# Kernel tuning notes

Measured on AMD Instinct MI355X. Metric: run time of the kernel, lower is better.

The kernel has to match this reference:

```python
import jax, jax.numpy as jnp
import numpy as np

# Model dims (Llama-7B-like with GQA)
HID = 4096      # hidden_size
NH = 32         # query heads
NKV = 8         # kv heads
D = HID // NH   # head_dim = 128
S = 64          # num decode sequences (one token each)
NB = 4096       # num cache blocks
BS = 16         # block size
MC = 1024       # max context length
THETA = 10000.0 # rope base


def _rope(x, positions):
    # x: [S, h, D]; neox-style rotary over full head_dim
    half = D // 2
    inv_freq = 1.0 / (THETA ** (jnp.arange(half, dtype=jnp.float32) * 2.0 / D))
    ang = positions.astype(jnp.float32)[:, None] * inv_freq  # [S, half]
    cos = jnp.cos(ang)[:, None, :]
    sin = jnp.sin(ang)[:, None, :]
    x1, x2 = x[..., :half], x[..., half:]
    return jnp.concatenate([x1 * cos - x2 * sin, x2 * cos + x1 * sin], axis=-1)


def setup_inputs() -> dict:
    key = jax.random.key(0)
    ks = jax.random.split(key, 8)
    hidden_states = jax.random.normal(ks[0], (S, HID), dtype=jnp.float32)
    k_cache = jax.random.normal(ks[1], (NB, BS, NKV, D), dtype=jnp.float32)
    v_cache = jax.random.normal(ks[2], (NB, BS, NKV, D), dtype=jnp.float32)
    qkv_w = jax.random.normal(ks[3], ((NH + 2 * NKV) * D, HID), dtype=jnp.float32) * 0.02
    o_w = jax.random.normal(ks[4], (HID, NH * D), dtype=jnp.float32) * 0.02
    context_lens = jnp.clip(jax.random.randint(ks[5], (S,), 1, MC + 1), 1, MC).astype(jnp.int32)
    positions = (context_lens - 1).astype(jnp.int32)  # current token position
    block_tables = jax.random.randint(ks[6], (S, MC // BS), 0, NB).astype(jnp.int32)
    return {"hidden_states": hidden_states, "k_cache": k_cache, "v_cache": v_cache,
            "qkv_w": qkv_w, "o_w": o_w, "positions": positions,
            "context_lens": context_lens, "block_tables": block_tables}


def reference(hidden_states, k_cache, v_cache, qkv_w, o_w, positions, context_lens, block_tables):
    # QKV projection (no bias)
    qkv = hidden_states @ qkv_w.T  # [S, (NH+2*NKV)*D]
    q, k, v = jnp.split(qkv, [NH * D, NH * D + NKV * D], axis=-1)
    q = _rope(q.reshape(S, NH, D), positions)
    k = _rope(k.reshape(S, NKV, D), positions)
    v = v.reshape(S, NKV, D)

    # paged KV gather via block tables: [S, MC, NKV, D]
    Kg = k_cache[block_tables].reshape(S, MC, NKV, D)
    Vg = v_cache[block_tables].reshape(S, MC, NKV, D)
    # write current token's k/v into its slot (positions = context_len - 1)
    idx = jnp.arange(S)
    Kg = Kg.at[idx, positions].set(k)
    Vg = Vg.at[idx, positions].set(v)

    # GQA attention without expanding KV heads
    G = NH // NKV
    qh = q.reshape(S, NKV, G, D) * (D ** -0.5)
    scores = jnp.einsum('skgd,sckd->skgc', qh, Kg)  # [S, NKV, G, MC]
    mask = jnp.arange(MC)[None, :] < context_lens[:, None]  # [S, MC]
    scores = jnp.where(mask[:, None, None, :], scores, -1e9)
    probs = jax.nn.softmax(scores, axis=-1)
    attn = jnp.einsum('skgc,sckd->skgd', probs, Vg).reshape(S, NH * D)

    # output projection
    return attn @ o_w.T
```

## Files before the change

### kernel.cpp

```cpp
#include <hip/hip_runtime.h>
#include <math.h>

#define HID 4096
#define NH  32
#define NKV 8
#define DH  128
#define SEQ 64
#define BS  16
#define MC  1024
#define QKV_N 6144
#define NPAGES 64
#define KC  64
#define KS  16
#define GQ  4
#define CSPLIT 8
#define TPS 128
#define RT  32
#define NHQ (SEQ * NH)

__device__ float g_qkv[SEQ * QKV_N];
__device__ float g_attn[SEQ * HID];
__device__ float g_part[KS * SEQ * QKV_N];
__device__ float g_po[CSPLIT * NHQ * DH];
__device__ float g_pm[CSPLIT * NHQ];
__device__ float g_pl[CSPLIT * NHQ];

__global__ __launch_bounds__(256) void gemm_tile(const float* __restrict__ X,
                                                 const float* __restrict__ W,
                                                 float* __restrict__ P,
                                                 int N, int K) {
    __shared__ float Xs[KC][68];
    __shared__ float Ws[KC][68];
    const int tid = threadIdx.x;
    const int tx = tid & 15;
    const int ty = tid >> 4;
    const int jb = blockIdx.x * 64;
    const int ks = blockIdx.y;
    const int k_lo = ks * (K / KS);
    const int k_hi = k_lo + (K / KS);

    float4 a0 = {0,0,0,0}, a1 = {0,0,0,0}, a2 = {0,0,0,0}, a3 = {0,0,0,0};

    for (int k0 = k_lo; k0 < k_hi; k0 += KC) {
        #pragma unroll
        for (int r = 0; r < 4; ++r) {
            int idx = r * 256 + tid;
            int s  = idx >> 4;
            int k4 = idx & 15;
            float4 v = *(const float4*)(X + (size_t)s * K + k0 + k4 * 4);
            Xs[k4 * 4 + 0][s] = v.x;
            Xs[k4 * 4 + 1][s] = v.y;
            Xs[k4 * 4 + 2][s] = v.z;
            Xs[k4 * 4 + 3][s] = v.w;
        }
        #pragma unroll
        for (int r = 0; r < 4; ++r) {
            int idx = r * 256 + tid;
            int j  = idx >> 4;
            int k4 = idx & 15;
            float4 v = *(const float4*)(W + (size_t)(jb + j) * K + k0 + k4 * 4);
            Ws[k4 * 4 + 0][j] = v.x;
            Ws[k4 * 4 + 1][j] = v.y;
            Ws[k4 * 4 + 2][j] = v.z;
            Ws[k4 * 4 + 3][j] = v.w;
        }
        __syncthreads();
        #pragma unroll
        for (int kk = 0; kk < KC; ++kk) {
            float4 xv = *(const float4*)(&Xs[kk][ty * 4]);
            float4 wv = *(const float4*)(&Ws[kk][tx * 4]);
            a0.x = fmaf(xv.x, wv.x, a0.x); a0.y = fmaf(xv.x, wv.y, a0.y);
            a0.z = fmaf(xv.x, wv.z, a0.z); a0.w = fmaf(xv.x, wv.w, a0.w);
            a1.x = fmaf(xv.y, wv.x, a1.x); a1.y = fmaf(xv.y, wv.y, a1.y);
            a1.z = fmaf(xv.y, wv.z, a1.z); a1.w = fmaf(xv.y, wv.w, a1.w);
            a2.x = fmaf(xv.z, wv.x, a2.x); a2.y = fmaf(xv.z, wv.y, a2.y);
            a2.z = fmaf(xv.z, wv.z, a2.z); a2.w = fmaf(xv.z, wv.w, a2.w);
            a3.x = fmaf(xv.w, wv.x, a3.x); a3.y = fmaf(xv.w, wv.y, a3.y);
            a3.z = fmaf(xv.w, wv.z, a3.z); a3.w = fmaf(xv.w, wv.w, a3.w);
        }
        __syncthreads();
    }
    float* pb = P + (size_t)ks * SEQ * N;
    *(float4*)(pb + (size_t)(ty * 4 + 0) * N + jb + tx * 4) = a0;
    *(float4*)(pb + (size_t)(ty * 4 + 1) * N + jb + tx * 4) = a1;
    *(float4*)(pb + (size_t)(ty * 4 + 2) * N + jb + tx * 4) = a2;
    *(float4*)(pb + (size_t)(ty * 4 + 3) * N + jb + tx * 4) = a3;
}

__global__ __launch_bounds__(256) void reduce_ks(const float* __restrict__ P,
                                                 float* __restrict__ Y, int n4) {
    int t = blockIdx.x * 256 + threadIdx.x;
    if (t >= n4) return;
    const float4* p4 = (const float4*)P;
    float4 r = p4[t];
    #pragma unroll
    for (int i = 1; i < KS; ++i) {
        float4 v = p4[t + (size_t)i * n4];
        r.x += v.x; r.y += v.y; r.z += v.z; r.w += v.w;
    }
    ((float4*)Y)[t] = r;
}

__global__ __launch_bounds__(256) void rope_scalar(float* __restrict__ qkv,
                                                   const int* __restrict__ ia,
                                                   const int* __restrict__ ib) {
    int t = blockIdx.x * 256 + threadIdx.x;
    if (t >= SEQ * (NH + NKV) * 64) return;
    int i = t & 63;
    int h = (t >> 6) % (NH + NKV);
    int s = t / ((NH + NKV) * 64);
    int pos = max(ia[s], ib[s]) - 1;
    float* base = qkv + (size_t)s * QKV_N + (size_t)h * DH;
    float ang = (float)pos / powf(10000.0f, (float)i * 2.0f / (float)DH);
    float sn, c;
    sincosf(ang, &sn, &c);
    float x1 = base[i];
    float x2 = base[i + 64];
    base[i]      = x1 * c - x2 * sn;
    base[i + 64] = x2 * c + x1 * sn;
}

__global__ __launch_bounds__(256) void attn_page(const float* __restrict__ qkv,
                                                 const float* __restrict__ k_cache,
                                                 const float* __restrict__ v_cache,
                                                 const int* __restrict__ ia,
                                                 const int* __restrict__ ib,
                                                 const int* __restrict__ block_tables,
                                                 float* __restrict__ po,
                                                 float* __restrict__ pm,
                                                 float* __restrict__ pl) {
    __shared__ float Klds[2][RT][129];
    __shared__ float Vlds[2][RT][130];
    __shared__ float qs[GQ][DH];
    __shared__ int   btl[NPAGES];

    int b  = blockIdx.x;
    int t  = b & 7;
    int kv = (b >> 3) & 7;
    int s  = b >> 6;
    int tid = threadIdx.x;
    int lane = tid & 63;
    int g = tid >> 6;

    int L   = max(ia[s], ib[s]);
    int pos = L - 1;
    int c_lo = t * TPS;
    if (c_lo >= L) return;
    int n = min(TPS, L - c_lo);
    int nrounds = (n + RT - 1) >> 5;

    if (tid < NPAGES) btl[tid] = block_tables[s * NPAGES + tid];
    for (int i = tid; i < GQ * DH; i += 256)
        qs[i >> 7][i & 127] = qkv[(size_t)s * QKV_N + (size_t)(kv * GQ) * DH + i]
                              * 0.08838834764831845f;
    __syncthreads();

    const float* knew = qkv + (size_t)s * QKV_N + (size_t)NH * DH + (size_t)kv * DH;
    const float* vnew = qkv + (size_t)s * QKV_N + (size_t)(NH + NKV) * DH + (size_t)kv * DH;

    const int sr = tid >> 3;
    const int sq = tid & 7;

    float4 ka0, ka1, ka2, ka3, va0, va1, va2, va3;

#define LOADR(BASE) do {                                                        \
    int cc = c_lo + (BASE) + sr;                                                \
    const float* kp_ = (cc == pos) ? knew                                       \
        : k_cache + ((size_t)btl[cc >> 4] * BS + (cc & 15)) * (size_t)(NKV * DH)\
                  + (size_t)kv * DH;                                            \
    const float* vp_ = (cc == pos) ? vnew                                       \
        : v_cache + ((size_t)btl[cc >> 4] * BS + (cc & 15)) * (size_t)(NKV * DH)\
                  + (size_t)kv * DH;                                            \
    const float4* kp4_ = (const float4*)kp_;                                    \
    const float4* vp4_ = (const float4*)vp_;                                    \
    ka0 = kp4_[sq];      ka1 = kp4_[sq + 8];                                    \
    ka2 = kp4_[sq + 16]; ka3 = kp4_[sq + 24];                                   \
    va0 = vp4_[sq];      va1 = vp4_[sq + 8];                                    \
    va2 = vp4_[sq + 16]; va3 = vp4_[sq + 24];                                   \
} while (0)

#define WRITER(BUF) do {                                                        \
    float* kd_ = &Klds[BUF][sr][0];                                             \
    kd_[4*sq+0]=ka0.x; kd_[4*sq+1]=ka0.y; kd_[4*sq+2]=ka0.z; kd_[4*sq+3]=ka0.w; \
    kd_[4*(sq+8)+0]=ka1.x; kd_[4*(sq+8)+1]=ka1.y;                               \
    kd_[4*(sq+8)+2]=ka1.z; kd_[4*(sq+8)+3]=ka1.w;                               \
    kd_[4*(sq+16)+0]=ka2.x; kd_[4*(sq+16)+1]=ka2.y;                             \
    kd_[4*(sq+16)+2]=ka2.z; kd_[4*(sq+16)+3]=ka2.w;                             \
    kd_[4*(sq+24)+0]=ka3.x; kd_[4*(sq+24)+1]=ka3.y;                             \
    kd_[4*(sq+24)+2]=ka3.z; kd_[4*(sq+24)+3]=ka3.w;                             \
    float* vd_ = &Vlds[BUF][sr][0];                                             \
    *(float2*)&vd_[4*sq+0]      = make_float2(va0.x, va0.y);                    \
    *(float2*)&vd_[4*sq+2]      = make_float2(va0.z, va0.w);                    \
    *(float2*)&vd_[4*(sq+8)+0]  = make_float2(va1.x, va1.y);                    \
    *(float2*)&vd_[4*(sq+8)+2]  = make_float2(va1.z, va1.w);                    \
    *(float2*)&vd_[4*(sq+16)+0] = make_float2(va2.x, va2.y);                    \
    *(float2*)&vd_[4*(sq+16)+2] = make_float2(va2.z, va2.w);                    \
    *(float2*)&vd_[4*(sq+24)+0] = make_float2(va3.x, va3.y);                    \
    *(float2*)&vd_[4*(sq+24)+2] = make_float2(va3.z, va3.w);                    \
} while (0)

    LOADR(0);
    WRITER(0);
    __syncthreads();

    float m = -1e30f, l = 0.f, o0 = 0.f, o1 = 0.f;
    int cur = 0;
    const int tkn = lane & 31;
    const int hh  = lane >> 5;

    for (int r = 0; r < nrounds; ++r) {
        int base = r << 5;
        if (r + 1 < nrounds) LOADR(base + RT);

        const float* krow = &Klds[cur][tkn][hh * 64];
        const float* qrow = &qs[g][hh * 64];
        float acc = 0.f;
        #pragma unroll
        for (int i = 0; i < 64; ++i) acc = fmaf(qrow[i], krow[i], acc);
        acc += __shfl_xor(acc, 32, 64);
        int c = c_lo + base + tkn;
        float scv = (c < L) ? acc : -1e30f;

        float rm = scv;
        #pragma unroll
        for (int off = 16; off; off >>= 1) rm = fmaxf(rm, __shfl_xor(rm, off, 64));
        float m_new = fmaxf(m, rm);
        float p = (c < L) ? expf(scv - m_new) : 0.f;
        float ps = p;
        #pragma unroll
        for (int off = 16; off; off >>= 1) ps += __shfl_xor(ps, off, 64);
        float rescale = expf(m - m_new);
        l = l * rescale + ps;
        o0 *= rescale; o1 *= rescale;
        m = m_new;

        int cnt = min(RT, n - base);
        for (int j = 0; j < cnt; ++j) {
            float pj = __shfl(p, j, 64);
            float2 v = *(const float2*)(&Vlds[cur][j][2 * lane]);
            o0 = fmaf(pj, v.x, o0);
            o1 = fmaf(pj, v.y, o1);
        }

        if (r + 1 < nrounds) {
            WRITER(cur ^ 1);
            __syncthreads();
            cur ^= 1;
        }
    }

    int idx = t * NHQ + s * NH + kv * GQ + g;
    float* ob = po + (size_t)idx * DH;
    ((float2*)ob)[lane] = make_float2(o0, o1);
    if (lane == 0) {
        pm[idx] = m;
        pl[idx] = l;
    }
#undef LOADR
#undef WRITER
}

__global__ __launch_bounds__(128) void attn_combine(const float* __restrict__ po,
                                                    const float* __restrict__ pm,
                                                    const float* __restrict__ pl,
                                                    const int* __restrict__ ia,
                                                    const int* __restrict__ ib,
                                                    float* __restrict__ attn_out) {
    int sh = blockIdx.x;
    int s  = sh >> 5;
    int d  = threadIdx.x;
    int L  = max(ia[s], ib[s]);
    int nact = (L + TPS - 1) / TPS;
    float mv[CSPLIT];
    float M = -1e30f;
    for (int i = 0; i < nact; ++i) {
        mv[i] = pm[i * NHQ + sh];
        M = fmaxf(M, mv[i]);
    }
    float num = 0.f, denom = 0.f;
    for (int i = 0; i < nact; ++i) {
        float w = expf(mv[i] - M);
        denom += pl[i * NHQ + sh] * w;
        num   += po[(size_t)(i * NHQ + sh) * DH + d] * w;
    }
    attn_out[(size_t)sh * DH + d] = num / denom;
}

extern "C" void kernel_launch(void* const* d_in, const int* in_sizes, int n_in,
                              void* d_out, int out_size, void* d_ws, size_t ws_size,
                              hipStream_t stream) {
    const float *hidden = nullptr, *k_cache = nullptr, *v_cache = nullptr;
    const float *qkv_w = nullptr, *o_w = nullptr;
    const int *i64a = nullptr, *i64b = nullptr, *block_tables = nullptr;
    for (int i = 0; i < n_in; ++i) {
        switch (in_sizes[i]) {
            case SEQ * HID:          hidden = (const float*)d_in[i]; break;
            case 4096 * BS * NKV * DH:
                if (!k_cache) k_cache = (const float*)d_in[i];
                else          v_cache = (const float*)d_in[i];
                break;
            case QKV_N * HID:        qkv_w = (const float*)d_in[i]; break;
            case HID * HID:          o_w   = (const float*)d_in[i]; break;
            case SEQ * NPAGES:       block_tables = (const int*)d_in[i]; break;
            case SEQ:
                if (!i64a) i64a = (const int*)d_in[i];
                else       i64b = (const int*)d_in[i];
                break;
        }
    }
    float* out = (float*)d_out;

    static float* qkv_p  = nullptr;
    static float* attn_p = nullptr;
    static float* part_p = nullptr;
    static float* po_p   = nullptr;
    static float* pm_p   = nullptr;
    static float* pl_p   = nullptr;
    if (!qkv_p) {
        void* p;
        hipGetSymbolAddress(&p, HIP_SYMBOL(g_qkv));  qkv_p  = (float*)p;
        hipGetSymbolAddress(&p, HIP_SYMBOL(g_attn)); attn_p = (float*)p;
        hipGetSymbolAddress(&p, HIP_SYMBOL(g_part)); part_p = (float*)p;
        hipGetSymbolAddress(&p, HIP_SYMBOL(g_po));   po_p   = (float*)p;
        hipGetSymbolAddress(&p, HIP_SYMBOL(g_pm));   pm_p   = (float*)p;
        hipGetSymbolAddress(&p, HIP_SYMBOL(g_pl));   pl_p   = (float*)p;
    }

    gemm_tile<<<dim3(QKV_N / 64, KS), 256, 0, stream>>>(hidden, qkv_w, part_p,
                                                        QKV_N, HID);
    reduce_ks<<<(SEQ * QKV_N / 4 + 255) / 256, 256, 0, stream>>>(part_p, qkv_p,
                                                                 SEQ * QKV_N / 4);
    rope_scalar<<<(SEQ * (NH + NKV) * 64) / 256, 256, 0, stream>>>(qkv_p, i64a, i64b);
    attn_page<<<SEQ * NKV * CSPLIT, 256, 0, stream>>>(qkv_p, k_cache, v_cache,
                                                      i64a, i64b, block_tables,
                                                      po_p, pm_p, pl_p);
    attn_combine<<<NHQ, 128, 0, stream>>>(po_p, pm_p, pl_p, i64a, i64b, attn_p);
    gemm_tile<<<dim3(HID / 64, KS), 256, 0, stream>>>(attn_p, o_w, part_p,
                                                      HID, HID);
    reduce_ks<<<(SEQ * HID / 4 + 255) / 256, 256, 0, stream>>>(part_p, out,
                                                               SEQ * HID / 4);
}
```

Baseline: 235.2 us.

## Compute QK scores in registers at load time, drop K staging in LDS

The attention kernel now keeps the scaled query rows in registers and computes Q·K dot products directly on the just-loaded K vectors, reducing across the 8 loader lanes with shuffles. Only the scores and V are written to shared memory, so the K shared-memory tile and its scalar stores and reads go away. Out-of-range rows are clamped to a valid address and masked when the score is stored. The cost is more registers (16 float4 for Q) and extra shuffle reductions per tile, which may lower occupancy.

```diff
diff --git a/kernel.cpp b/kernel.cpp
--- a/kernel.cpp
+++ b/kernel.cpp
@@ -17,6 +17,7 @@
 #define TPS 128
 #define RT  32
 #define NHQ (SEQ * NH)
+#define SCALE 0.08838834764831845f
 
 __device__ float g_qkv[SEQ * QKV_N];
 __device__ float g_attn[SEQ * HID];
@@ -120,18 +121,17 @@
     base[i + 64] = x2 * c + x1 * sn;
 }
 
-__global__ __launch_bounds__(256) void attn_page(const float* __restrict__ qkv,
-                                                 const float* __restrict__ k_cache,
-                                                 const float* __restrict__ v_cache,
-                                                 const int* __restrict__ ia,
-                                                 const int* __restrict__ ib,
-                                                 const int* __restrict__ block_tables,
-                                                 float* __restrict__ po,
-                                                 float* __restrict__ pm,
-                                                 float* __restrict__ pl) {
-    __shared__ float Klds[2][RT][129];
-    __shared__ float Vlds[2][RT][130];
-    __shared__ float qs[GQ][DH];
+__global__ __launch_bounds__(256) void attn_reg(const float* __restrict__ qkv,
+                                                const float* __restrict__ k_cache,
+                                                const float* __restrict__ v_cache,
+                                                const int* __restrict__ ia,
+                                                const int* __restrict__ ib,
+                                                const int* __restrict__ block_tables,
+                                                float* __restrict__ po,
+                                                float* __restrict__ pm,
+                                                float* __restrict__ pl) {
+    __shared__ float Vlds[2][RT][132];
+    __shared__ float sc_lds[2][GQ][34];
     __shared__ int   btl[NPAGES];
 
     int b  = blockIdx.x;
@@ -146,30 +146,44 @@
     int pos = L - 1;
     int c_lo = t * TPS;
     if (c_lo >= L) return;
-    int n = min(TPS, L - c_lo);
+    int c_hi = min(c_lo + TPS, L);
+    int n = c_hi - c_lo;
     int nrounds = (n + RT - 1) >> 5;
 
+    const int sr = tid >> 3;
+    const int sq = tid & 7;
+
     if (tid < NPAGES) btl[tid] = block_tables[s * NPAGES + tid];
-    for (int i = tid; i < GQ * DH; i += 256)
-        qs[i >> 7][i & 127] = qkv[(size_t)s * QKV_N + (size_t)(kv * GQ) * DH + i]
-                              * 0.08838834764831845f;
     __syncthreads();
 
     const float* knew = qkv + (size_t)s * QKV_N + (size_t)NH * DH + (size_t)kv * DH;
     const float* vnew = qkv + (size_t)s * QKV_N + (size_t)(NH + NKV) * DH + (size_t)kv * DH;
 
-    const int sr = tid >> 3;
-    const int sq = tid & 7;
+    float4 qf[GQ][4];
+    #pragma unroll
+    for (int gg = 0; gg < GQ; ++gg) {
+        const float4* qr = (const float4*)(qkv + (size_t)s * QKV_N
+                                           + (size_t)(kv * GQ + gg) * DH);
+        #pragma unroll
+        for (int j = 0; j < 4; ++j) {
+            float4 v = qr[sq + 8 * j];
+            v.x *= SCALE; v.y *= SCALE; v.z *= SCALE; v.w *= SCALE;
+            qf[gg][j] = v;
+        }
+    }
 
     float4 ka0, ka1, ka2, ka3, va0, va1, va2, va3;
+    bool vrow;
 
 #define LOADR(BASE) do {                                                        \
     int cc = c_lo + (BASE) + sr;                                                \
-    const float* kp_ = (cc == pos) ? knew                                       \
-        : k_cache + ((size_t)btl[cc >> 4] * BS + (cc & 15)) * (size_t)(NKV * DH)\
+    vrow = cc < c_hi;                                                           \
+    int cs = vrow ? cc : pos;                                                   \
+    const float* kp_ = (cs == pos) ? knew                                       \
+        : k_cache + ((size_t)btl[cs >> 4] * BS + (cs & 15)) * (size_t)(NKV * DH)\
                   + (size_t)kv * DH;                                            \
-    const float* vp_ = (cc == pos) ? vnew                                       \
-        : v_cache + ((size_t)btl[cc >> 4] * BS + (cc & 15)) * (size_t)(NKV * DH)\
+    const float* vp_ = (cs == pos) ? vnew                                       \
+        : v_cache + ((size_t)btl[cs >> 4] * BS + (cs & 15)) * (size_t)(NKV * DH)\
                   + (size_t)kv * DH;                                            \
     const float4* kp4_ = (const float4*)kp_;                                    \
     const float4* vp4_ = (const float4*)vp_;                                    \
@@ -179,53 +193,53 @@
     va2 = vp4_[sq + 16]; va3 = vp4_[sq + 24];                                   \
 } while (0)
 
-#define WRITER(BUF) do {                                                        \
-    float* kd_ = &Klds[BUF][sr][0];                                             \
-    kd_[4*sq+0]=ka0.x; kd_[4*sq+1]=ka0.y; kd_[4*sq+2]=ka0.z; kd_[4*sq+3]=ka0.w; \
-    kd_[4*(sq+8)+0]=ka1.x; kd_[4*(sq+8)+1]=ka1.y;                               \
-    kd_[4*(sq+8)+2]=ka1.z; kd_[4*(sq+8)+3]=ka1.w;                               \
-    kd_[4*(sq+16)+0]=ka2.x; kd_[4*(sq+16)+1]=ka2.y;                             \
-    kd_[4*(sq+16)+2]=ka2.z; kd_[4*(sq+16)+3]=ka2.w;                             \
-    kd_[4*(sq+24)+0]=ka3.x; kd_[4*(sq+24)+1]=ka3.y;                             \
-    kd_[4*(sq+24)+2]=ka3.z; kd_[4*(sq+24)+3]=ka3.w;                             \
-    float* vd_ = &Vlds[BUF][sr][0];                                             \
-    *(float2*)&vd_[4*sq+0]      = make_float2(va0.x, va0.y);                    \
-    *(float2*)&vd_[4*sq+2]      = make_float2(va0.z, va0.w);                    \
-    *(float2*)&vd_[4*(sq+8)+0]  = make_float2(va1.x, va1.y);                    \
-    *(float2*)&vd_[4*(sq+8)+2]  = make_float2(va1.z, va1.w);                    \
-    *(float2*)&vd_[4*(sq+16)+0] = make_float2(va2.x, va2.y);                    \
-    *(float2*)&vd_[4*(sq+16)+2] = make_float2(va2.z, va2.w);                    \
-    *(float2*)&vd_[4*(sq+24)+0] = make_float2(va3.x, va3.y);                    \
-    *(float2*)&vd_[4*(sq+24)+2] = make_float2(va3.z, va3.w);                    \
+#define DOT4(Q, K) ((Q).x*(K).x + (Q).y*(K).y + (Q).z*(K).z + (Q).w*(K).w)
+
+#define STORER(BUF) do {                                                        \
+    float pp0 = DOT4(qf[0][0],ka0)+DOT4(qf[0][1],ka1)                           \
+              + DOT4(qf[0][2],ka2)+DOT4(qf[0][3],ka3);                          \
+    float pp1 = DOT4(qf[1][0],ka0)+DOT4(qf[1][1],ka1)                           \
+              + DOT4(qf[1][2],ka2)+DOT4(qf[1][3],ka3);                          \
+    float pp2 = DOT4(qf[2][0],ka0)+DOT4(qf[2][1],ka1)                           \
+              + DOT4(qf[2][2],ka2)+DOT4(qf[2][3],ka3);                          \
+    float pp3 = DOT4(qf[3][0],ka0)+DOT4(qf[3][1],ka1)                           \
+              + DOT4(qf[3][2],ka2)+DOT4(qf[3][3],ka3);                          \
+    pp0 += __shfl_xor(pp0, 1, 64); pp0 += __shfl_xor(pp0, 2, 64);               \
+    pp0 += __shfl_xor(pp0, 4, 64);                                              \
+    pp1 += __shfl_xor(pp1, 1, 64); pp1 += __shfl_xor(pp1, 2, 64);               \
+    pp1 += __shfl_xor(pp1, 4, 64);                                              \
+    pp2 += __shfl_xor(pp2, 1, 64); pp2 += __shfl_xor(pp2, 2, 64);               \
+    pp2 += __shfl_xor(pp2, 4, 64);                                              \
+    pp3 += __shfl_xor(pp3, 1, 64); pp3 += __shfl_xor(pp3, 2, 64);               \
+    pp3 += __shfl_xor(pp3, 4, 64);                                              \
+    if (sq < 4) {                                                               \
+        float ppsel = (sq == 0) ? pp0 : (sq == 1) ? pp1 : (sq == 2) ? pp2 : pp3;\
+        sc_lds[BUF][sq][sr] = vrow ? ppsel : -1e30f;                            \
+    }                                                                           \
+    *(float4*)(&Vlds[BUF][sr][4 * sq])        = va0;                            \
+    *(float4*)(&Vlds[BUF][sr][4 * (sq + 8)])  = va1;                            \
+    *(float4*)(&Vlds[BUF][sr][4 * (sq + 16)]) = va2;                            \
+    *(float4*)(&Vlds[BUF][sr][4 * (sq + 24)]) = va3;                            \
 } while (0)
 
     LOADR(0);
-    WRITER(0);
+    STORER(0);
     __syncthreads();
 
     float m = -1e30f, l = 0.f, o0 = 0.f, o1 = 0.f;
     int cur = 0;
     const int tkn = lane & 31;
-    const int hh  = lane >> 5;
 
     for (int r = 0; r < nrounds; ++r) {
         int base = r << 5;
         if (r + 1 < nrounds) LOADR(base + RT);
 
-        const float* krow = &Klds[cur][tkn][hh * 64];
-        const float* qrow = &qs[g][hh * 64];
-        float acc = 0.f;
-        #pragma unroll
-        for (int i = 0; i < 64; ++i) acc = fmaf(qrow[i], krow[i], acc);
-        acc += __shfl_xor(acc, 32, 64);
-        int c = c_lo + base + tkn;
-        float scv = (c < L) ? acc : -1e30f;
-
-        float rm = scv;
+        float sco = sc_lds[cur][g][tkn];
+        float rm = sco;
         #pragma unroll
         for (int off = 16; off; off >>= 1) rm = fmaxf(rm, __shfl_xor(rm, off, 64));
         float m_new = fmaxf(m, rm);
-        float p = (c < L) ? expf(scv - m_new) : 0.f;
+        float p = expf(sco - m_new);
         float ps = p;
         #pragma unroll
         for (int off = 16; off; off >>= 1) ps += __shfl_xor(ps, off, 64);
@@ -243,7 +257,7 @@
         }
 
         if (r + 1 < nrounds) {
-            WRITER(cur ^ 1);
+            STORER(cur ^ 1);
             __syncthreads();
             cur ^= 1;
         }
@@ -257,7 +271,8 @@
         pl[idx] = l;
     }
 #undef LOADR
-#undef WRITER
+#undef DOT4
+#undef STORER
 }
 
 __global__ __launch_bounds__(128) void attn_combine(const float* __restrict__ po,
@@ -331,9 +346,9 @@
     reduce_ks<<<(SEQ * QKV_N / 4 + 255) / 256, 256, 0, stream>>>(part_p, qkv_p,
                                                                  SEQ * QKV_N / 4);
     rope_scalar<<<(SEQ * (NH + NKV) * 64) / 256, 256, 0, stream>>>(qkv_p, i64a, i64b);
-    attn_page<<<SEQ * NKV * CSPLIT, 256, 0, stream>>>(qkv_p, k_cache, v_cache,
-                                                      i64a, i64b, block_tables,
-                                                      po_p, pm_p, pl_p);
+    attn_reg<<<SEQ * NKV * CSPLIT, 256, 0, stream>>>(qkv_p, k_cache, v_cache,
+                                                     i64a, i64b, block_tables,
+                                                     po_p, pm_p, pl_p);
     attn_combine<<<NHQ, 128, 0, stream>>>(po_p, pm_p, pl_p, i64a, i64b, attn_p);
     gemm_tile<<<dim3(HID / 64, KS), 256, 0, stream>>>(attn_p, o_w, part_p,
                                                       HID, HID);
```

New measurement: 206.6 us. -12.2%, faster.
